# Performance work log

Hardware: AMD Instinct MI355X
Metric: run time of the kernel (lower is better)

Reference implementation:

```python
import jax, jax.numpy as jnp
import numpy as np
from jax import lax

PADDING = 1  # from init_kwargs; must equal (k-1)//2 so the residual add is shape-valid


def _conv_single(x, w):
    # x: [C_in, H, W], w: [C_out, C_in, kH, kW] -> [C_out, H, W]
    y = lax.conv_general_dilated(
        x[None],  # [1, C_in, H, W]
        w,
        window_strides=(1, 1),
        padding=[(PADDING, PADDING), (PADDING, PADDING)],
        dimension_numbers=("NCHW", "OIHW", "NCHW"),
    )
    return y[0]


def setup_inputs() -> dict:
    key = jax.random.key(0)
    k1, k2 = jax.random.split(key)
    B, C, H, W, K = 16, 128, 64, 64, 3
    inp = jax.random.normal(k1, (B, C, H, W), dtype=jnp.float32)
    # per-sample dynamic weights, scaled so conv output is O(1)
    weight = jax.random.normal(k2, (B, C, C, K, K), dtype=jnp.float32) * (1.0 / np.sqrt(C * K * K))
    return {"input": inp, "weight": weight}


def reference(input, weight):
    # per-sample conv2d with a different kernel per batch element + residual add
    residual = jax.vmap(_conv_single)(input, weight)  # [B, C, H, W]
    return input + residual
```

## Files before the change

### kernel.cpp

```cpp
#include <hip/hip_runtime.h>
#include <hip/hip_bf16.h>


typedef _Float16 h8 __attribute__((ext_vector_type(8)));
typedef _Float16 h4 __attribute__((ext_vector_type(4)));
typedef float f32x16 __attribute__((ext_vector_type(16)));
typedef float f4 __attribute__((ext_vector_type(4)));

#define MFMA32 __builtin_amdgcn_mfma_f32_32x32x16_f16

__global__ __launch_bounds__(256) void w_prepass(const float* __restrict__ W,
                                                 _Float16* __restrict__ wp) {
    __shared__ float raw[8 * 1153];
    const int bid = blockIdx.x;
    const int b   = bid >> 4;
    const int co0 = (bid & 15) * 8;
    const int t   = threadIdx.x;

    const float* src = W + (size_t)(b * 128 + co0) * 1152;
#pragma unroll
    for (int i = 0; i < 9; ++i) {
        int idx  = (i * 256 + t) * 4;
        f4 v     = *(const f4*)(src + idx);
        int co_l = idx / 1152;
        int rem  = idx - co_l * 1152;
        *(f4*)&raw[co_l * 1153 + rem] = v;
    }
    __syncthreads();

#pragma unroll
    for (int i = 0; i < 9; ++i) {
        int c    = i * 256 + t;
        int jh   = c & 1;
        int co_l = (c >> 1) & 7;
        int oct  = (c >> 4) & 3;
        int r    = c >> 6;
        int kw   = r % 3;
        int r2   = r / 3;
        int kc   = r2 & 3;
        int kh   = r2 >> 2;
        int cib  = kc * 32 + oct * 8 + jh * 4;
        h4 v;
#pragma unroll
        for (int jj = 0; jj < 4; ++jj)
            v[jj] = (_Float16)raw[co_l * 1153 + (cib + jj) * 9 + kh * 3 + kw];
        size_t o = ((size_t)(b * 3 + kh) * 4 + kc) * 12288 +
                   (size_t)(kw * 4 + oct) * 1024 + (size_t)(co0 + co_l) * 8 + jh * 4;
        *(h4*)&wp[o] = v;
    }
}


__global__ __launch_bounds__(256, 2) void conv_main(const float* __restrict__ X,
                                                    const _Float16* __restrict__ wp,
                                                    float* __restrict__ out) {
    __shared__ _Float16 sX[2 * 4224];

    const int t    = threadIdx.x;
    const int lane = t & 63;
    const int l31  = lane & 31;
    const int lhi  = lane >> 5;
    const int wv   = t >> 6;
    const int wvM  = wv >> 1;
    const int wr   = wv & 1;

    const int bid   = blockIdx.x;
    const int swz   = (bid & 7) * 64 + (bid >> 3);
    const int batch = swz >> 5;
    const int h0    = (swz & 31) * 2;

    const int sy  = t >> 7;
    const int xq  = (t & 15) * 4;
    const int cio = (t >> 4) & 7;

    f32x16 acc[2][2];
#pragma unroll
    for (int mt = 0; mt < 2; ++mt)
#pragma unroll
        for (int nt = 0; nt < 2; ++nt)
#pragma unroll
            for (int r = 0; r < 16; ++r) acc[mt][nt][r] = 0.f;

    if (t < 32) {
        int pb = t >> 4, y = (t >> 3) & 1, oct = (t >> 1) & 3, side = t & 1;
        h8 z = {};
        *(h8*)&sX[pb * 4224 + ((y * 4 + oct) * 66 + side * 65) * 8] = z;
    }

    f4 xrv[4];

    const int wrow = (lhi * 128 + wvM * 64 + l31) * 8;

    auto load_x = [&](int s) {
        const int kh = s >> 2, kc = s & 3;
        const int yy = h0 + sy + kh - 1;
        if (yy >= 0 && yy < 64) {
            const float* xp = X + ((size_t)(batch * 128 + kc * 32 + cio * 4) * 64 + yy) * 64 + xq;
#pragma unroll
            for (int j = 0; j < 4; ++j) xrv[j] = *(const f4*)(xp + (size_t)j * 4096);
        } else {
#pragma unroll
            for (int j = 0; j < 4; ++j) xrv[j] = (f4){0.f, 0.f, 0.f, 0.f};
        }
    };

    auto write_x = [&](int pb) {
#pragma unroll
        for (int k = 0; k < 4; ++k) {
            h4 v = {(_Float16)xrv[0][k], (_Float16)xrv[1][k],
                    (_Float16)xrv[2][k], (_Float16)xrv[3][k]};
            *(h4*)&sX[pb * 4224 + ((sy * 4 + (cio >> 1)) * 66 + xq + 1 + k) * 8 + (cio & 1) * 4] = v;
        }
    };

    auto compute = [&](int s, int pb) {
        const int kh = s >> 2, kc = s & 3;
        const _Float16* wbase = wp + ((size_t)(batch * 3 + kh) * 4 + kc) * 12288 + wrow;
        const _Float16* sXp = sX + pb * 4224;
#pragma unroll
        for (int ks = 0; ks < 6; ++ks) {
            const int kw = ks >> 1, kk = ks & 1;
            h8 af[2], bf[2];
#pragma unroll
            for (int mt = 0; mt < 2; ++mt)
                af[mt] = *(const h8*)&wbase[(size_t)((kw * 4 + kk * 2) * 128 + mt * 32) * 8];
#pragma unroll
            for (int nt = 0; nt < 2; ++nt)
                bf[nt] = *(const h8*)&sXp[((wr * 4 + kk * 2 + lhi) * 66 + nt * 32 + l31 + kw) * 8];
            __builtin_amdgcn_s_setprio(1);
#pragma unroll
            for (int mt = 0; mt < 2; ++mt)
#pragma unroll
                for (int nt = 0; nt < 2; ++nt)
                    acc[mt][nt] = MFMA32(af[mt], bf[nt], acc[mt][nt], 0, 0, 0);
            __builtin_amdgcn_s_setprio(0);
        }
    };

    load_x(0);
    write_x(0);
    __syncthreads();

    int p = 0;
#pragma unroll 1
    for (int s = 0; s < 11; ++s) {
        load_x(s + 1);
        compute(s, p);
        write_x(p ^ 1);
        __syncthreads();
        p ^= 1;
    }
    compute(11, p);

#pragma unroll
    for (int mt = 0; mt < 2; ++mt)
#pragma unroll
        for (int nt = 0; nt < 2; ++nt)
#pragma unroll
            for (int rg = 0; rg < 16; ++rg) {
                int co = wvM * 64 + mt * 32 + (rg & 3) + 8 * (rg >> 2) + 4 * lhi;
                int x  = nt * 32 + l31;
                size_t o = ((size_t)(batch * 128 + co) * 64 + h0 + wr) * 64 + x;
                out[o] = X[o] + acc[mt][nt][rg];
            }
}

extern "C" void kernel_launch(void* const* d_in, const int* in_sizes, int n_in,
                              void* d_out, int out_size, void* d_ws, size_t ws_size,
                              hipStream_t stream) {
    const float* inp = (const float*)d_in[0];
    const float* wgt = (const float*)d_in[1];
    float* out = (float*)d_out;
    _Float16* wpk = (_Float16*)d_ws;

    w_prepass<<<256, 256, 0, stream>>>(wgt, wpk);
    conv_main<<<512, 256, 0, stream>>>(inp, wpk, out);
}
```

Measured before the change: 120.6 us.

## Shrink conv tile to one output row per block and raise occupancy

Each block of the main conv kernel now computes a single output row with each wave owning 32 output channels, instead of two rows with a 64-channel-per-wave tile. The grid doubles to 1024 blocks, shared memory halves and launch bounds rise to 4 blocks per SM, aiming to improve occupancy and latency hiding. The cost is less reuse per block: each weight fragment now feeds only two MFMAs instead of four, so weight traffic from global/L2 roughly doubles, and input rows are reloaded more often. The prepass also replaces its vectorized h4 store with scalar half stores.

```diff
diff --git a/kernel.cpp b/kernel.cpp
--- a/kernel.cpp
+++ b/kernel.cpp
@@ -3,7 +3,7 @@
 
 
 typedef _Float16 h8 __attribute__((ext_vector_type(8)));
-typedef _Float16 h4 __attribute__((ext_vector_type(4)));
+typedef _Float16 h2 __attribute__((ext_vector_type(2)));
 typedef float f32x16 __attribute__((ext_vector_type(16)));
 typedef float f4 __attribute__((ext_vector_type(4)));
 
@@ -40,99 +40,91 @@
         int kc   = r2 & 3;
         int kh   = r2 >> 2;
         int cib  = kc * 32 + oct * 8 + jh * 4;
-        h4 v;
-#pragma unroll
-        for (int jj = 0; jj < 4; ++jj)
-            v[jj] = (_Float16)raw[co_l * 1153 + (cib + jj) * 9 + kh * 3 + kw];
+        _Float16 v0 = (_Float16)raw[co_l * 1153 + (cib + 0) * 9 + kh * 3 + kw];
+        _Float16 v1 = (_Float16)raw[co_l * 1153 + (cib + 1) * 9 + kh * 3 + kw];
+        _Float16 v2 = (_Float16)raw[co_l * 1153 + (cib + 2) * 9 + kh * 3 + kw];
+        _Float16 v3 = (_Float16)raw[co_l * 1153 + (cib + 3) * 9 + kh * 3 + kw];
         size_t o = ((size_t)(b * 3 + kh) * 4 + kc) * 12288 +
                    (size_t)(kw * 4 + oct) * 1024 + (size_t)(co0 + co_l) * 8 + jh * 4;
-        *(h4*)&wp[o] = v;
+        wp[o + 0] = v0; wp[o + 1] = v1; wp[o + 2] = v2; wp[o + 3] = v3;
     }
 }
 
 
-__global__ __launch_bounds__(256, 2) void conv_main(const float* __restrict__ X,
+__global__ __launch_bounds__(256, 4) void conv_main(const float* __restrict__ X,
                                                     const _Float16* __restrict__ wp,
                                                     float* __restrict__ out) {
-    __shared__ _Float16 sX[2 * 4224];
+    __shared__ _Float16 sX[2 * 2112];
 
     const int t    = threadIdx.x;
     const int lane = t & 63;
     const int l31  = lane & 31;
     const int lhi  = lane >> 5;
     const int wv   = t >> 6;
-    const int wvM  = wv >> 1;
-    const int wr   = wv & 1;
 
     const int bid   = blockIdx.x;
-    const int swz   = (bid & 7) * 64 + (bid >> 3);
-    const int batch = swz >> 5;
-    const int h0    = (swz & 31) * 2;
+    const int swz   = (bid & 7) * 128 + (bid >> 3);
+    const int batch = swz >> 6;
+    const int h     = swz & 63;
 
-    const int sy  = t >> 7;
-    const int xq  = (t & 15) * 4;
-    const int cio = (t >> 4) & 7;
+    const int p  = t >> 4;
+    const int xq = (t & 15) * 4;
 
-    f32x16 acc[2][2];
+    f32x16 acc[2];
 #pragma unroll
-    for (int mt = 0; mt < 2; ++mt)
+    for (int nt = 0; nt < 2; ++nt)
 #pragma unroll
-        for (int nt = 0; nt < 2; ++nt)
-#pragma unroll
-            for (int r = 0; r < 16; ++r) acc[mt][nt][r] = 0.f;
+        for (int r = 0; r < 16; ++r) acc[nt][r] = 0.f;
 
-    if (t < 32) {
-        int pb = t >> 4, y = (t >> 3) & 1, oct = (t >> 1) & 3, side = t & 1;
+    if (t < 16) {
+        int pb = t >> 3, oct = (t >> 1) & 3, side = t & 1;
         h8 z = {};
-        *(h8*)&sX[pb * 4224 + ((y * 4 + oct) * 66 + side * 65) * 8] = z;
+        *(h8*)&sX[pb * 2112 + (oct * 66 + side * 65) * 8] = z;
     }
 
-    f4 xrv[4];
+    f4 xa, xb;
 
-    const int wrow = (lhi * 128 + wvM * 64 + l31) * 8;
+    const int wrow = (lhi * 128 + wv * 32 + l31) * 8;
 
     auto load_x = [&](int s) {
         const int kh = s >> 2, kc = s & 3;
-        const int yy = h0 + sy + kh - 1;
+        const int yy = h + kh - 1;
         if (yy >= 0 && yy < 64) {
-            const float* xp = X + ((size_t)(batch * 128 + kc * 32 + cio * 4) * 64 + yy) * 64 + xq;
-#pragma unroll
-            for (int j = 0; j < 4; ++j) xrv[j] = *(const f4*)(xp + (size_t)j * 4096);
+            const float* xp = X + ((size_t)(batch * 128 + kc * 32 + 2 * p) * 64 + yy) * 64 + xq;
+            xa = *(const f4*)xp;
+            xb = *(const f4*)(xp + 4096);
         } else {
-#pragma unroll
-            for (int j = 0; j < 4; ++j) xrv[j] = (f4){0.f, 0.f, 0.f, 0.f};
+            xa = (f4){0.f, 0.f, 0.f, 0.f};
+            xb = (f4){0.f, 0.f, 0.f, 0.f};
         }
     };
 
     auto write_x = [&](int pb) {
+        const int oct = p >> 2;
+        const int sub = (p & 3) * 2;
 #pragma unroll
         for (int k = 0; k < 4; ++k) {
-            h4 v = {(_Float16)xrv[0][k], (_Float16)xrv[1][k],
-                    (_Float16)xrv[2][k], (_Float16)xrv[3][k]};
-            *(h4*)&sX[pb * 4224 + ((sy * 4 + (cio >> 1)) * 66 + xq + 1 + k) * 8 + (cio & 1) * 4] = v;
+            h2 v = {(_Float16)xa[k], (_Float16)xb[k]};
+            *(h2*)&sX[pb * 2112 + (oct * 66 + xq + 1 + k) * 8 + sub] = v;
         }
     };
 
     auto compute = [&](int s, int pb) {
         const int kh = s >> 2, kc = s & 3;
         const _Float16* wbase = wp + ((size_t)(batch * 3 + kh) * 4 + kc) * 12288 + wrow;
-        const _Float16* sXp = sX + pb * 4224;
+        const _Float16* sXp = sX + pb * 2112;
 #pragma unroll
         for (int ks = 0; ks < 6; ++ks) {
             const int kw = ks >> 1, kk = ks & 1;
-            h8 af[2], bf[2];
-#pragma unroll
-            for (int mt = 0; mt < 2; ++mt)
-                af[mt] = *(const h8*)&wbase[(size_t)((kw * 4 + kk * 2) * 128 + mt * 32) * 8];
+            h8 af, bf[2];
+            af = *(const h8*)&wbase[(size_t)((kw * 4 + kk * 2) * 128) * 8];
 #pragma unroll
             for (int nt = 0; nt < 2; ++nt)
-                bf[nt] = *(const h8*)&sXp[((wr * 4 + kk * 2 + lhi) * 66 + nt * 32 + l31 + kw) * 8];
+                bf[nt] = *(const h8*)&sXp[((kk * 2 + lhi) * 66 + nt * 32 + l31 + kw) * 8];
             __builtin_amdgcn_s_setprio(1);
 #pragma unroll
-            for (int mt = 0; mt < 2; ++mt)
-#pragma unroll
-                for (int nt = 0; nt < 2; ++nt)
-                    acc[mt][nt] = MFMA32(af[mt], bf[nt], acc[mt][nt], 0, 0, 0);
+            for (int nt = 0; nt < 2; ++nt)
+                acc[nt] = MFMA32(af, bf[nt], acc[nt], 0, 0, 0);
             __builtin_amdgcn_s_setprio(0);
         }
     };
@@ -141,28 +133,26 @@
     write_x(0);
     __syncthreads();
 
-    int p = 0;
+    int pbuf = 0;
 #pragma unroll 1
     for (int s = 0; s < 11; ++s) {
         load_x(s + 1);
-        compute(s, p);
-        write_x(p ^ 1);
+        compute(s, pbuf);
+        write_x(pbuf ^ 1);
         __syncthreads();
-        p ^= 1;
+        pbuf ^= 1;
     }
-    compute(11, p);
+    compute(11, pbuf);
 
 #pragma unroll
-    for (int mt = 0; mt < 2; ++mt)
+    for (int nt = 0; nt < 2; ++nt)
 #pragma unroll
-        for (int nt = 0; nt < 2; ++nt)
-#pragma unroll
-            for (int rg = 0; rg < 16; ++rg) {
-                int co = wvM * 64 + mt * 32 + (rg & 3) + 8 * (rg >> 2) + 4 * lhi;
-                int x  = nt * 32 + l31;
-                size_t o = ((size_t)(batch * 128 + co) * 64 + h0 + wr) * 64 + x;
-                out[o] = X[o] + acc[mt][nt][rg];
-            }
+        for (int rg = 0; rg < 16; ++rg) {
+            int co = wv * 32 + (rg & 3) + 8 * (rg >> 2) + 4 * lhi;
+            int x  = nt * 32 + l31;
+            size_t o = ((size_t)(batch * 128 + co) * 64 + h) * 64 + x;
+            out[o] = X[o] + acc[nt][rg];
+        }
 }
 
 extern "C" void kernel_launch(void* const* d_in, const int* in_sizes, int n_in,
@@ -174,5 +164,5 @@
     _Float16* wpk = (_Float16*)d_ws;
 
     w_prepass<<<256, 256, 0, stream>>>(wgt, wpk);
-    conv_main<<<512, 256, 0, stream>>>(inp, wpk, out);
+    conv_main<<<1024, 256, 0, stream>>>(inp, wpk, out);
 }
```

After: 117.7 us. 2.4% less time.
